# Optimization experiments

Measured on AMD Instinct MI355X. Metric: run time of the kernel, lower is better.

Reference implementation:

```python
import jax, jax.numpy as jnp
import numpy as np
import math

B, S_IN, S_OUT, D_IN, D_OUT, G = 8, 1024, 1024, 96, 96, 8
LN_EPS = 1e-5


def setup_inputs() -> dict:
    key = jax.random.key(0)
    k_x, k_m, k_p, k_l = jax.random.split(key, 4)
    x = jax.random.normal(k_x, (B, S_IN, D_IN), dtype=jnp.float32)
    M = jax.random.uniform(k_m, (D_OUT, D_IN), minval=-0.5, maxval=0.5, dtype=jnp.float32)
    P = jax.random.uniform(k_p, (D_OUT, D_OUT, G), minval=-0.1, maxval=0.1, dtype=jnp.float32)
    Linker = jax.random.uniform(k_l, (S_IN, S_OUT), minval=-0.1, maxval=0.1, dtype=jnp.float32)
    gamma = jnp.ones((D_OUT,), dtype=jnp.float32)
    beta = jnp.zeros((D_OUT,), dtype=jnp.float32)
    return {"x": x, "M": M, "P": P, "Linker": Linker, "gamma": gamma, "beta": beta}


def _layer_norm(z, gamma, beta):
    mu = jnp.mean(z, axis=-1, keepdims=True)
    var = jnp.mean(jnp.square(z - mu), axis=-1, keepdims=True)
    return (z - mu) * jax.lax.rsqrt(var + LN_EPS) * gamma + beta


def reference(x, M, P, Linker, gamma, beta):
    # Z = x @ M^T, then LayerNorm over feature dim
    Z0 = jnp.einsum('bsj,ij->bsi', x, M)           # (B, S_in, D_out)
    Z = _layer_norm(Z0, gamma, beta)
    # periods[i,j,g] = i*(D_out*G) + j*G + g + 2
    periods = (jnp.arange(D_OUT * D_OUT * G, dtype=jnp.float32)
               .reshape(D_OUT, D_OUT, G) + 2.0)
    k = jnp.arange(S_IN, dtype=jnp.float32)
    # phi[s,i,j,g] = cos(2*pi*s / periods[i,j,g])
    phi = jnp.cos((2.0 * math.pi) * k[:, None, None, None] / periods[None])
    # fuse basis reduction: W[s,i,j] = sum_g P[i,j,g] * phi[s,i,j,g]
    W = jnp.einsum('sijg,ijg->sij', phi, P)        # (S_in, D_out, D_out)
    # T[b,s,i] = sum_j Z[b,s,j] * W[s,i,j]
    T = jnp.einsum('bsj,sij->bsi', Z, W)           # (B, S_in, D_out)
    # sequence transform via Linker
    U = jnp.einsum('bsi,st->bti', T, Linker)       # (B, S_out, D_out)
    # shared residual: x @ M^T (pre-LN) through the same Linker
    residual = jnp.einsum('bsi,st->bti', Z0, Linker)
    return U + residual
```

## Files before the change

kernel.cpp:

```cpp
#include <hip/hip_runtime.h>
#include <cstdint>
#include <cstddef>

#define NPAIR 9216
#define BSTRIDE 98304

typedef __attribute__((ext_vector_type(8))) short short8;
typedef __attribute__((ext_vector_type(4))) float f32x4;

__device__ __forceinline__ uint16_t f2bf(float x) {
    uint32_t u = __float_as_uint(x);
    return (uint16_t)((u + 0x7FFF + ((u >> 16) & 1)) >> 16);
}
__device__ __forceinline__ float bf2f(uint16_t b) {
    return __uint_as_float(((uint32_t)b) << 16);
}

union SmemK1 {
    float M[96][97];
    struct { float zb[16][100]; float ps[16][6][2]; float stats[16][2]; } ln;
    struct { float T[64][65]; } kl;
};

__global__ __launch_bounds__(96) void k1_mega(
    const float* __restrict__ x, const float* __restrict__ M,
    const float* __restrict__ P, const float* __restrict__ L,
    const float* __restrict__ gamma, const float* __restrict__ beta,
    float* __restrict__ Z0, float* __restrict__ Z,
    uint16_t* __restrict__ Lt, uint16_t* __restrict__ Wt)
{
    __shared__ SmemK1 sm;
    const int t  = threadIdx.x;
    const int bx = blockIdx.x;

    if (bx < 512) {
        const int R0 = bx * 16;
        for (int k = 0; k < 24; ++k) {
            int mm = t + 96 * k;
            int i = mm / 24, j0 = (mm % 24) * 4;
            float4 v = *(const float4*)(M + i * 96 + j0);
            sm.M[i][j0]   = v.x; sm.M[i][j0+1] = v.y;
            sm.M[i][j0+2] = v.z; sm.M[i][j0+3] = v.w;
        }
        __syncthreads();
        float mreg[96];
        #pragma unroll
        for (int j = 0; j < 96; ++j) mreg[j] = sm.M[t][j];
        __syncthreads();

        for (int r = 0; r < 16; ++r) {
            const float* xr = x + (size_t)(R0 + r) * 96;
            float a0 = 0.f, a1 = 0.f, a2 = 0.f, a3 = 0.f;
            #pragma unroll
            for (int j = 0; j < 96; j += 4) {
                a0 = fmaf(xr[j+0], mreg[j+0], a0);
                a1 = fmaf(xr[j+1], mreg[j+1], a1);
                a2 = fmaf(xr[j+2], mreg[j+2], a2);
                a3 = fmaf(xr[j+3], mreg[j+3], a3);
            }
            float z = (a0 + a1) + (a2 + a3);
            sm.ln.zb[r][t] = z;
            Z0[(size_t)(R0 + r) * 96 + t] = z;
        }
        __syncthreads();
        {
            const int row = t / 6, seg = t % 6;
            const float4* zp = (const float4*)&sm.ln.zb[row][seg * 16];
            float s1 = 0.f, s2 = 0.f;
            #pragma unroll
            for (int k = 0; k < 4; ++k) {
                float4 v = zp[k];
                s1 += v.x + v.y + v.z + v.w;
                s2 += v.x*v.x + v.y*v.y + v.z*v.z + v.w*v.w;
            }
            sm.ln.ps[row][seg][0] = s1;
            sm.ln.ps[row][seg][1] = s2;
        }
        __syncthreads();
        if (t < 16) {
            float s1 = 0.f, s2 = 0.f;
            #pragma unroll
            for (int k = 0; k < 6; ++k) {
                s1 += sm.ln.ps[t][k][0];
                s2 += sm.ln.ps[t][k][1];
            }
            float mu  = s1 * (1.f / 96.f);
            float var = s2 * (1.f / 96.f) - mu * mu;
            sm.ln.stats[t][0] = mu;
            sm.ln.stats[t][1] = rsqrtf(var + 1e-5f);
        }
        __syncthreads();
        {
            float gm = gamma[t], bt = beta[t];
            for (int r = 0; r < 16; ++r) {
                float mu = sm.ln.stats[r][0], rs = sm.ln.stats[r][1];
                Z[(size_t)(R0 + r) * 96 + t] =
                    (sm.ln.zb[r][t] - mu) * rs * gm + bt;
            }
        }
        return;
    }

    if (bx < 768) {
        const int bx2 = bx - 512;
        const int s0 = (bx2 & 15) * 64, t0 = (bx2 >> 4) * 64;
        if (t < 64) {
            for (int r = 0; r < 64; ++r)
                sm.kl.T[r][t] = L[(size_t)(s0 + r) * 1024 + t0 + t];
        }
        __syncthreads();
        if (t < 64) {
            uint16_t* orow = Lt + (size_t)(t0 + t) * 1024 + s0;
            #pragma unroll
            for (int c4 = 0; c4 < 16; ++c4) {
                uint32_t u01 = (uint32_t)f2bf(sm.kl.T[c4*4+0][t]) |
                               ((uint32_t)f2bf(sm.kl.T[c4*4+1][t]) << 16);
                uint32_t u23 = (uint32_t)f2bf(sm.kl.T[c4*4+2][t]) |
                               ((uint32_t)f2bf(sm.kl.T[c4*4+3][t]) << 16);
                uint2 o; o.x = u01; o.y = u23;
                *(uint2*)(orow + c4 * 4) = o;
            }
        }
        return;
    }

    {
        const int idx = bx - 768;
        const int pb  = idx % 96;
        const int sc  = idx / 96;
        const int p   = pb * 96 + t;
        const int i   = p % 96, j = p / 96;
        const int s0  = sc * 64;
        const int base = (i * 96 + j) * 8;

        float Pv[8], c[8], cp[8], tc1[8];
        {
            float4 a = *(const float4*)(P + base);
            float4 b = *(const float4*)(P + base + 4);
            Pv[0]=a.x; Pv[1]=a.y; Pv[2]=a.z; Pv[3]=a.w;
            Pv[4]=b.x; Pv[5]=b.y; Pv[6]=b.z; Pv[7]=b.w;
        }
        #pragma unroll
        for (int g = 0; g < 8; ++g) {
            float inv = 1.0f / (float)(base + g + 2);
            float c1  = cospif(2.0f * inv);
            tc1[g] = c1 + c1;
            c[g]  = cospif(2.0f * (float)s0 * inv);
            cp[g] = cospif(2.0f * (float)(s0 - 1) * inv);
        }
        uint16_t* op = Wt + (size_t)s0 * NPAIR + p;
        for (int ss = 0; ss < 64; ++ss) {
            float w = 0.f;
            #pragma unroll
            for (int g = 0; g < 8; ++g) w = fmaf(Pv[g], c[g], w);
            *op = f2bf(w);
            op += NPAIR;
            #pragma unroll
            for (int g = 0; g < 8; ++g) {
                float cn = fmaf(tc1[g], c[g], -cp[g]);
                cp[g] = c[g]; c[g] = cn;
            }
        }
    }
}

__global__ __launch_bounds__(96) void kt_apply(
    const float* __restrict__ Z, const float* __restrict__ Z0,
    const uint16_t* __restrict__ Wt, uint16_t* __restrict__ Vt)
{
    const int i = threadIdx.x;
    const int s = blockIdx.x;
    float acc[8] = {0.f,0.f,0.f,0.f,0.f,0.f,0.f,0.f};
    const uint16_t* wrow = Wt + (size_t)s * NPAIR + i;
    const float* zs = Z + (size_t)s * 96;
    #pragma unroll 8
    for (int j = 0; j < 96; ++j) {
        float w = bf2f(wrow[j * 96]);
        #pragma unroll
        for (int bb = 0; bb < 8; ++bb)
            acc[bb] = fmaf(zs[(size_t)bb * BSTRIDE + j], w, acc[bb]);
    }
    #pragma unroll
    for (int bb = 0; bb < 8; ++bb) {
        size_t o = (size_t)bb * BSTRIDE + (size_t)s * 96 + i;
        Vt[((size_t)bb * 96 + i) * 1024 + s] = f2bf(acc[bb] + Z0[o]);
    }
}

__global__ __launch_bounds__(128) void k3_mfma(
    const uint16_t* __restrict__ Lt, const uint16_t* __restrict__ Vt,
    float* __restrict__ out)
{
    const int lane = threadIdx.x & 63;
    const int wv   = threadIdx.x >> 6;
    const int m    = lane & 15;
    const int quad = lane >> 4;
    const int t0   = blockIdx.x * 32 + wv * 16;
    const int b    = blockIdx.y;

    const uint16_t* Lp = Lt + (size_t)(t0 + m) * 1024 + quad * 8;
    const uint16_t* Vp = Vt + ((size_t)b * 96 + m) * 1024 + quad * 8;

    f32x4 acc[6];
    #pragma unroll
    for (int ii = 0; ii < 6; ++ii) acc[ii] = (f32x4){0.f, 0.f, 0.f, 0.f};

    short8 a = *(const short8*)Lp;
    short8 bv[6];
    #pragma unroll
    for (int ii = 0; ii < 6; ++ii)
        bv[ii] = *(const short8*)(Vp + (size_t)ii * 16 * 1024);

    for (int kc = 0; kc < 31; ++kc) {
        short8 an = *(const short8*)(Lp + (kc + 1) * 32);
        short8 bn[6];
        #pragma unroll
        for (int ii = 0; ii < 6; ++ii)
            bn[ii] = *(const short8*)(Vp + (size_t)ii * 16 * 1024 + (kc + 1) * 32);
        #pragma unroll
        for (int ii = 0; ii < 6; ++ii)
            acc[ii] = __builtin_amdgcn_mfma_f32_16x16x32_bf16(a, bv[ii], acc[ii], 0, 0, 0);
        a = an;
        #pragma unroll
        for (int ii = 0; ii < 6; ++ii) bv[ii] = bn[ii];
    }
    #pragma unroll
    for (int ii = 0; ii < 6; ++ii)
        acc[ii] = __builtin_amdgcn_mfma_f32_16x16x32_bf16(a, bv[ii], acc[ii], 0, 0, 0);

    float* po = out + (size_t)b * BSTRIDE;
    #pragma unroll
    for (int ii = 0; ii < 6; ++ii)
        #pragma unroll
        for (int r = 0; r < 4; ++r)
            po[(size_t)(t0 + quad * 4 + r) * 96 + ii * 16 + m] = acc[ii][r];
}

extern "C" void kernel_launch(void* const* d_in, const int* in_sizes, int n_in,
                              void* d_out, int out_size, void* d_ws, size_t ws_size,
                              hipStream_t stream)
{
    const float* x     = (const float*)d_in[0];
    const float* M     = (const float*)d_in[1];
    const float* P     = (const float*)d_in[2];
    const float* Lnk   = (const float*)d_in[3];
    const float* gamma = (const float*)d_in[4];
    const float* beta  = (const float*)d_in[5];
    float* out = (float*)d_out;

    uint8_t* ws = (uint8_t*)d_ws;
    uint16_t* Wt = (uint16_t*)ws;
    float*    Z0 = (float*)(ws + 18874368);
    float*    Z  = (float*)(ws + 22020096);
    uint16_t* Lt = (uint16_t*)(ws + 25165824);
    uint16_t* Vt = (uint16_t*)(ws + 27262976);

    k1_mega <<<2304, 96, 0, stream>>>(x, M, P, Lnk, gamma, beta, Z0, Z, Lt, Wt);
    kt_apply<<<1024, 96, 0, stream>>>(Z, Z0, Wt, Vt);
    k3_mfma <<<dim3(32, 8), 128, 0, stream>>>(Lt, Vt, out);
}
```

Before: 124.8 us.

## Fuse projection, LayerNorm, W generation and apply into one per-sequence kernel

Merges the x@M^T projection, LayerNorm, on-the-fly W basis generation and the per-position apply into a single kernel with one block per sequence position. W is kept in shared memory instead of a 18MB bf16 workspace, and Z/Z0 are no longer written to global memory. The cosine is now evaluated directly with hardware rcp/cos on range-reduced arguments rather than by a Chebyshev recurrence, and the MFMA GEMM splits K across two wave pairs with a shared-memory reduction. Each block now recomputes 9216×8 cosines, which adds transcendental work per block, and the hardware cos carries lower accuracy.

```diff
diff --git a/kernel.cpp b/kernel.cpp
--- a/kernel.cpp
+++ b/kernel.cpp
@@ -2,7 +2,6 @@
 #include <cstdint>
 #include <cstddef>
 
-#define NPAIR 9216
 #define BSTRIDE 98304
 
 typedef __attribute__((ext_vector_type(8))) short short8;
@@ -16,93 +15,30 @@
     return __uint_as_float(((uint32_t)b) << 16);
 }
 
-union SmemK1 {
-    float M[96][97];
-    struct { float zb[16][100]; float ps[16][6][2]; float stats[16][2]; } ln;
+union SmemF {
+    struct {
+        float    xs[8][96];
+        float    zs[96][8];
+        uint16_t W[96][98];
+        float    ps1[8][12];
+        float    ps2[8][12];
+        float    stats[8][2];
+    } f;
     struct { float T[64][65]; } kl;
 };
 
-__global__ __launch_bounds__(96) void k1_mega(
+__global__ __launch_bounds__(96) void k_fused(
     const float* __restrict__ x, const float* __restrict__ M,
     const float* __restrict__ P, const float* __restrict__ L,
     const float* __restrict__ gamma, const float* __restrict__ beta,
-    float* __restrict__ Z0, float* __restrict__ Z,
-    uint16_t* __restrict__ Lt, uint16_t* __restrict__ Wt)
+    uint16_t* __restrict__ Lt, uint16_t* __restrict__ Vt)
 {
-    __shared__ SmemK1 sm;
+    __shared__ SmemF sm;
     const int t  = threadIdx.x;
     const int bx = blockIdx.x;
 
-    if (bx < 512) {
-        const int R0 = bx * 16;
-        for (int k = 0; k < 24; ++k) {
-            int mm = t + 96 * k;
-            int i = mm / 24, j0 = (mm % 24) * 4;
-            float4 v = *(const float4*)(M + i * 96 + j0);
-            sm.M[i][j0]   = v.x; sm.M[i][j0+1] = v.y;
-            sm.M[i][j0+2] = v.z; sm.M[i][j0+3] = v.w;
-        }
-        __syncthreads();
-        float mreg[96];
-        #pragma unroll
-        for (int j = 0; j < 96; ++j) mreg[j] = sm.M[t][j];
-        __syncthreads();
-
-        for (int r = 0; r < 16; ++r) {
-            const float* xr = x + (size_t)(R0 + r) * 96;
-            float a0 = 0.f, a1 = 0.f, a2 = 0.f, a3 = 0.f;
-            #pragma unroll
-            for (int j = 0; j < 96; j += 4) {
-                a0 = fmaf(xr[j+0], mreg[j+0], a0);
-                a1 = fmaf(xr[j+1], mreg[j+1], a1);
-                a2 = fmaf(xr[j+2], mreg[j+2], a2);
-                a3 = fmaf(xr[j+3], mreg[j+3], a3);
-            }
-            float z = (a0 + a1) + (a2 + a3);
-            sm.ln.zb[r][t] = z;
-            Z0[(size_t)(R0 + r) * 96 + t] = z;
-        }
-        __syncthreads();
-        {
-            const int row = t / 6, seg = t % 6;
-            const float4* zp = (const float4*)&sm.ln.zb[row][seg * 16];
-            float s1 = 0.f, s2 = 0.f;
-            #pragma unroll
-            for (int k = 0; k < 4; ++k) {
-                float4 v = zp[k];
-                s1 += v.x + v.y + v.z + v.w;
-                s2 += v.x*v.x + v.y*v.y + v.z*v.z + v.w*v.w;
-            }
-            sm.ln.ps[row][seg][0] = s1;
-            sm.ln.ps[row][seg][1] = s2;
-        }
-        __syncthreads();
-        if (t < 16) {
-            float s1 = 0.f, s2 = 0.f;
-            #pragma unroll
-            for (int k = 0; k < 6; ++k) {
-                s1 += sm.ln.ps[t][k][0];
-                s2 += sm.ln.ps[t][k][1];
-            }
-            float mu  = s1 * (1.f / 96.f);
-            float var = s2 * (1.f / 96.f) - mu * mu;
-            sm.ln.stats[t][0] = mu;
-            sm.ln.stats[t][1] = rsqrtf(var + 1e-5f);
-        }
-        __syncthreads();
-        {
-            float gm = gamma[t], bt = beta[t];
-            for (int r = 0; r < 16; ++r) {
-                float mu = sm.ln.stats[r][0], rs = sm.ln.stats[r][1];
-                Z[(size_t)(R0 + r) * 96 + t] =
-                    (sm.ln.zb[r][t] - mu) * rs * gm + bt;
-            }
-        }
-        return;
-    }
-
-    if (bx < 768) {
-        const int bx2 = bx - 512;
+    if (bx >= 1024) {
+        const int bx2 = bx - 1024;
         const int s0 = (bx2 & 15) * 64, t0 = (bx2 >> 4) * 64;
         if (t < 64) {
             for (int r = 0; r < 64; ++r)
@@ -124,82 +60,124 @@
         return;
     }
 
+    const int s = bx;
+
+    float mreg[96];
+    #pragma unroll
+    for (int j0 = 0; j0 < 96; j0 += 4) {
+        float4 v = *(const float4*)(M + (size_t)t * 96 + j0);
+        mreg[j0+0] = v.x; mreg[j0+1] = v.y; mreg[j0+2] = v.z; mreg[j0+3] = v.w;
+    }
+    #pragma unroll
+    for (int k = 0; k < 8; ++k)
+        sm.f.xs[k][t] = x[(size_t)k * BSTRIDE + (size_t)s * 96 + t];
+    __syncthreads();
+
+    float zacc[8];
+    #pragma unroll
+    for (int b = 0; b < 8; ++b) {
+        float a0 = 0.f, a1 = 0.f, a2 = 0.f, a3 = 0.f;
+        #pragma unroll
+        for (int j0 = 0; j0 < 96; j0 += 4) {
+            float4 v = *(const float4*)&sm.f.xs[b][j0];
+            a0 = fmaf(v.x, mreg[j0+0], a0);
+            a1 = fmaf(v.y, mreg[j0+1], a1);
+            a2 = fmaf(v.z, mreg[j0+2], a2);
+            a3 = fmaf(v.w, mreg[j0+3], a3);
+        }
+        zacc[b] = (a0 + a1) + (a2 + a3);
+    }
+    #pragma unroll
+    for (int b = 0; b < 8; ++b) sm.f.zs[t][b] = zacc[b];
+    __syncthreads();
+
     {
-        const int idx = bx - 768;
-        const int pb  = idx % 96;
-        const int sc  = idx / 96;
-        const int p   = pb * 96 + t;
-        const int i   = p % 96, j = p / 96;
-        const int s0  = sc * 64;
-        const int base = (i * 96 + j) * 8;
-
-        float Pv[8], c[8], cp[8], tc1[8];
-        {
-            float4 a = *(const float4*)(P + base);
-            float4 b = *(const float4*)(P + base + 4);
-            Pv[0]=a.x; Pv[1]=a.y; Pv[2]=a.z; Pv[3]=a.w;
-            Pv[4]=b.x; Pv[5]=b.y; Pv[6]=b.z; Pv[7]=b.w;
-        }
-        #pragma unroll
-        for (int g = 0; g < 8; ++g) {
-            float inv = 1.0f / (float)(base + g + 2);
-            float c1  = cospif(2.0f * inv);
-            tc1[g] = c1 + c1;
-            c[g]  = cospif(2.0f * (float)s0 * inv);
-            cp[g] = cospif(2.0f * (float)(s0 - 1) * inv);
-        }
-        uint16_t* op = Wt + (size_t)s0 * NPAIR + p;
-        for (int ss = 0; ss < 64; ++ss) {
+        const int b = t / 12, grp = t % 12;
+        float s1 = 0.f, s2 = 0.f;
+        #pragma unroll
+        for (int k = 0; k < 8; ++k) {
+            float v = sm.f.zs[grp * 8 + k][b];
+            s1 += v; s2 += v * v;
+        }
+        sm.f.ps1[b][grp] = s1; sm.f.ps2[b][grp] = s2;
+    }
+    __syncthreads();
+    if (t < 8) {
+        float s1 = 0.f, s2 = 0.f;
+        #pragma unroll
+        for (int k = 0; k < 12; ++k) { s1 += sm.f.ps1[t][k]; s2 += sm.f.ps2[t][k]; }
+        float mu  = s1 * (1.f / 96.f);
+        float var = s2 * (1.f / 96.f) - mu * mu;
+        sm.f.stats[t][0] = mu;
+        sm.f.stats[t][1] = rsqrtf(var + 1e-5f);
+    }
+    __syncthreads();
+    {
+        float gm = gamma[t], bt = beta[t];
+        #pragma unroll
+        for (int b = 0; b < 8; ++b)
+            sm.f.zs[t][b] = (zacc[b] - sm.f.stats[b][0]) * sm.f.stats[b][1] * gm + bt;
+    }
+
+    {
+        const float sf = (float)s;
+        const float* Pp = P + (size_t)t * 8;
+        float perf = (float)(t * 8 + 2);
+        #pragma unroll 2
+        for (int i = 0; i < 96; ++i) {
+            float4 pa = *(const float4*)(Pp + (size_t)i * 768);
+            float4 pb = *(const float4*)(Pp + (size_t)i * 768 + 4);
+            float pv[8] = {pa.x, pa.y, pa.z, pa.w, pb.x, pb.y, pb.z, pb.w};
             float w = 0.f;
             #pragma unroll
-            for (int g = 0; g < 8; ++g) w = fmaf(Pv[g], c[g], w);
-            *op = f2bf(w);
-            op += NPAIR;
-            #pragma unroll
             for (int g = 0; g < 8; ++g) {
-                float cn = fmaf(tc1[g], c[g], -cp[g]);
-                cp[g] = c[g]; c[g] = cn;
+                float inv = __builtin_amdgcn_rcpf(perf + (float)g);
+                float a2  = sf * inv;
+                a2 -= floorf(a2);
+                w = fmaf(pv[g], __builtin_amdgcn_cosf(a2), w);
             }
-        }
-    }
-}
-
-__global__ __launch_bounds__(96) void kt_apply(
-    const float* __restrict__ Z, const float* __restrict__ Z0,
-    const uint16_t* __restrict__ Wt, uint16_t* __restrict__ Vt)
-{
-    const int i = threadIdx.x;
-    const int s = blockIdx.x;
-    float acc[8] = {0.f,0.f,0.f,0.f,0.f,0.f,0.f,0.f};
-    const uint16_t* wrow = Wt + (size_t)s * NPAIR + i;
-    const float* zs = Z + (size_t)s * 96;
-    #pragma unroll 8
+            sm.f.W[t][i] = f2bf(w);
+            perf += 768.0f;
+        }
+    }
+    __syncthreads();
+
+    float tacc[8] = {0.f,0.f,0.f,0.f,0.f,0.f,0.f,0.f};
+    #pragma unroll 4
     for (int j = 0; j < 96; ++j) {
-        float w = bf2f(wrow[j * 96]);
-        #pragma unroll
-        for (int bb = 0; bb < 8; ++bb)
-            acc[bb] = fmaf(zs[(size_t)bb * BSTRIDE + j], w, acc[bb]);
-    }
-    #pragma unroll
-    for (int bb = 0; bb < 8; ++bb) {
-        size_t o = (size_t)bb * BSTRIDE + (size_t)s * 96 + i;
-        Vt[((size_t)bb * 96 + i) * 1024 + s] = f2bf(acc[bb] + Z0[o]);
-    }
-}
-
-__global__ __launch_bounds__(128) void k3_mfma(
+        float w = bf2f(sm.f.W[j][t]);
+        float4 z0 = *(const float4*)&sm.f.zs[j][0];
+        float4 z1 = *(const float4*)&sm.f.zs[j][4];
+        tacc[0] = fmaf(z0.x, w, tacc[0]);
+        tacc[1] = fmaf(z0.y, w, tacc[1]);
+        tacc[2] = fmaf(z0.z, w, tacc[2]);
+        tacc[3] = fmaf(z0.w, w, tacc[3]);
+        tacc[4] = fmaf(z1.x, w, tacc[4]);
+        tacc[5] = fmaf(z1.y, w, tacc[5]);
+        tacc[6] = fmaf(z1.z, w, tacc[6]);
+        tacc[7] = fmaf(z1.w, w, tacc[7]);
+    }
+    #pragma unroll
+    for (int b = 0; b < 8; ++b)
+        Vt[((size_t)b * 96 + t) * 1024 + s] = f2bf(tacc[b] + zacc[b]);
+}
+
+__global__ __launch_bounds__(256) void k3_mfma(
     const uint16_t* __restrict__ Lt, const uint16_t* __restrict__ Vt,
     float* __restrict__ out)
 {
+    __shared__ float racc[2][64][25];
     const int lane = threadIdx.x & 63;
     const int wv   = threadIdx.x >> 6;
+    const int tw   = wv & 1;
+    const int kw   = wv >> 1;
     const int m    = lane & 15;
     const int quad = lane >> 4;
-    const int t0   = blockIdx.x * 32 + wv * 16;
+    const int t0   = blockIdx.x * 32 + tw * 16;
     const int b    = blockIdx.y;
 
-    const uint16_t* Lp = Lt + (size_t)(t0 + m) * 1024 + quad * 8;
-    const uint16_t* Vp = Vt + ((size_t)b * 96 + m) * 1024 + quad * 8;
+    const uint16_t* Lp = Lt + (size_t)(t0 + m) * 1024 + kw * 512 + quad * 8;
+    const uint16_t* Vp = Vt + ((size_t)b * 96 + m) * 1024 + kw * 512 + quad * 8;
 
     f32x4 acc[6];
     #pragma unroll
@@ -211,7 +189,7 @@
     for (int ii = 0; ii < 6; ++ii)
         bv[ii] = *(const short8*)(Vp + (size_t)ii * 16 * 1024);
 
-    for (int kc = 0; kc < 31; ++kc) {
+    for (int kc = 0; kc < 15; ++kc) {
         short8 an = *(const short8*)(Lp + (kc + 1) * 32);
         short8 bn[6];
         #pragma unroll
@@ -228,12 +206,23 @@
     for (int ii = 0; ii < 6; ++ii)
         acc[ii] = __builtin_amdgcn_mfma_f32_16x16x32_bf16(a, bv[ii], acc[ii], 0, 0, 0);
 
-    float* po = out + (size_t)b * BSTRIDE;
-    #pragma unroll
-    for (int ii = 0; ii < 6; ++ii)
-        #pragma unroll
-        for (int r = 0; r < 4; ++r)
-            po[(size_t)(t0 + quad * 4 + r) * 96 + ii * 16 + m] = acc[ii][r];
+    if (kw == 1) {
+        #pragma unroll
+        for (int ii = 0; ii < 6; ++ii)
+            #pragma unroll
+            for (int r = 0; r < 4; ++r)
+                racc[tw][lane][ii * 4 + r] = acc[ii][r];
+    }
+    __syncthreads();
+    if (kw == 0) {
+        float* po = out + (size_t)b * BSTRIDE;
+        #pragma unroll
+        for (int ii = 0; ii < 6; ++ii)
+            #pragma unroll
+            for (int r = 0; r < 4; ++r)
+                po[(size_t)(t0 + quad * 4 + r) * 96 + ii * 16 + m] =
+                    acc[ii][r] + racc[tw][lane][ii * 4 + r];
+    }
 }
 
 extern "C" void kernel_launch(void* const* d_in, const int* in_sizes, int n_in,
@@ -249,13 +238,9 @@
     float* out = (float*)d_out;
 
     uint8_t* ws = (uint8_t*)d_ws;
-    uint16_t* Wt = (uint16_t*)ws;
-    float*    Z0 = (float*)(ws + 18874368);
-    float*    Z  = (float*)(ws + 22020096);
-    uint16_t* Lt = (uint16_t*)(ws + 25165824);
-    uint16_t* Vt = (uint16_t*)(ws + 27262976);
-
-    k1_mega <<<2304, 96, 0, stream>>>(x, M, P, Lnk, gamma, beta, Z0, Z, Lt, Wt);
-    kt_apply<<<1024, 96, 0, stream>>>(Z, Z0, Wt, Vt);
-    k3_mfma <<<dim3(32, 8), 128, 0, stream>>>(Lt, Vt, out);
-}
+    uint16_t* Lt = (uint16_t*)ws;
+    uint16_t* Vt = (uint16_t*)(ws + 2097152);
+
+    k_fused <<<1280, 96, 0, stream>>>(x, M, P, Lnk, gamma, beta, Lt, Vt);
+    k3_mfma <<<dim3(32, 8), 256, 0, stream>>>(Lt, Vt, out);
+}
```

After: 142.4 us. 1.14x slower.
